# Kernel tuning notes

Hardware: AMD Instinct MI355X
Metric: run time of the kernel (lower is better)

## Reference

```python
import jax, jax.numpy as jnp
import numpy as np

K_NEIGHBORS = 3  # self.K in DSVDD


def setup_inputs() -> dict:
    key = jax.random.key(0)
    k1, k2 = jax.random.split(key)
    B, N, C = 16, 3136, 112   # batch, h*w patches, descriptor channels
    M = 3136                  # memory-bank size
    phi_p = jax.random.normal(k1, (B, N, C), dtype=jnp.float32)
    C_bank = jax.random.normal(k2, (C, M), dtype=jnp.float32)
    return {"phi_p": phi_p, "C_bank": C_bank, "h": 56}


def reference(phi_p, C_bank, h):
    # squared distances via ||phi||^2 + ||c||^2 - 2 phi.c  -> (B, N, M)
    features = jnp.sum(phi_p * phi_p, axis=2, keepdims=True)        # (B, N, 1)
    centers = jnp.sum(C_bank * C_bank, axis=0, keepdims=True)       # (1, M)
    f_c = 2.0 * jnp.einsum('bnc,cm->bnm', phi_p, C_bank)            # (B, N, M)
    dist = jnp.sqrt(features + centers - f_c)                        # (B, N, M)
    # K smallest distances (ascending, like torch.topk(largest=False))
    neg_topk, _ = jax.lax.top_k(-dist, K_NEIGHBORS)                  # (B, N, K)
    dist_k = -neg_topk
    # softmin over K, take weight of the nearest neighbor times its distance
    softmin0 = jax.nn.softmax(-dist_k, axis=-1)[:, :, 0]             # (B, N)
    score = softmin0 * dist_k[:, :, 0]                               # (B, N)
    B, N = score.shape
    w = N // h
    return score.reshape(B, 1, h, w)  # b c h w with c=1
```

## Files before the change

### kernel.cpp

```cpp
#include <hip/hip_runtime.h>
#include <stdint.h>


typedef short s16x8 __attribute__((ext_vector_type(8)));
typedef float fx4 __attribute__((ext_vector_type(4)));

#define M_TOT 3136
#define CC 112
#define NROWS 50176
#define N_TILES_TOT 50

__device__ __forceinline__ unsigned short f2bf(float x) {
  unsigned u = __float_as_uint(x);
  u += 0x7fffu + ((u >> 16) & 1u);
  return (unsigned short)(u >> 16);
}

__device__ __forceinline__ void async16(const void* g, void* l) {
  __builtin_amdgcn_global_load_lds(
      (const __attribute__((address_space(1))) unsigned int*)g,
      (__attribute__((address_space(3))) unsigned int*)l, 16, 0, 0);
}

#define INSERT3(T0, T1, T2, V)                                  \
  do {                                                          \
    const float _a0 = (T0), _a1 = (T1), _v = (V);               \
    (T0) = fmaxf(_a0, _v);                                      \
    (T1) = __builtin_amdgcn_fmed3f(_a0, _a1, _v);               \
    (T2) = __builtin_amdgcn_fmed3f(_a1, (T2), _v);              \
  } while (0)

__global__ __launch_bounds__(256) void dsvdd_prep(const float* __restrict__ Cb,
                                                  unsigned char* __restrict__ CT2) {
  const int tile = blockIdx.x;
  __shared__ float partial[256];
  __shared__ float c2s[64];
  const int tm = threadIdx.x & 63;
  const int seg = threadIdx.x >> 6;
  const int m = tile * 64 + tm;
  float ss = 0.f;
  if (m < M_TOT) {
    for (int k = seg * 28; k < seg * 28 + 28; ++k) {
      const float x = Cb[(size_t)k * M_TOT + m];
      ss += x * x;
    }
  }
  partial[threadIdx.x] = ss;
  __syncthreads();
  if (seg == 0) {
    const float c2 = partial[tm] + partial[64 + tm] + partial[128 + tm] + partial[192 + tm];
    c2s[tm] = (m < M_TOT) ? (-0.125f * c2) : -2500.0f;
  }
  __syncthreads();
#pragma unroll
  for (int it = 0; it < 4; ++it) {
    const int s = it * 256 + threadIdx.x;
    const int f = s >> 8;
    const int ks = (s >> 6) & 3;
    const int l = s & 63;
    const int mloc = f * 16 + (l & 15);
    const int mm = tile * 64 + mloc;
    const bool mv = (mm < M_TOT);
    const int k0 = ks * 32 + (l >> 4) * 8;
    float v[8];
#pragma unroll
    for (int j = 0; j < 8; ++j) {
      const int k = k0 + j;
      float x = 0.f;
      if (k < CC) x = mv ? Cb[(size_t)k * M_TOT + mm] : 0.f;
      else if (k < 116) x = c2s[mloc];
      v[j] = x;
    }
    uint4 pk;
    pk.x = (unsigned)f2bf(v[0]) | ((unsigned)f2bf(v[1]) << 16);
    pk.y = (unsigned)f2bf(v[2]) | ((unsigned)f2bf(v[3]) << 16);
    pk.z = (unsigned)f2bf(v[4]) | ((unsigned)f2bf(v[5]) << 16);
    pk.w = (unsigned)f2bf(v[6]) | ((unsigned)f2bf(v[7]) << 16);
    *(uint4*)(CT2 + (size_t)tile * 16384 + (size_t)s * 16) = pk;
  }
}

__global__ __launch_bounds__(256, 4) void dsvdd_stage1(const float* __restrict__ phi,
                                                       const unsigned char* __restrict__ CT2,
                                                       float* __restrict__ part,
                                                       float* __restrict__ featg, int nT) {
  __shared__ __align__(16) unsigned char lds[32768];
  float(*const mg)[8] = (float(*)[8])lds;

  const int t = threadIdx.x;
  const int lane = t & 63;
  const int w = t >> 6;
  const int g = w >> 1;
  const int h = w & 1;
  const int cq = lane & 15;
  const int kq = lane >> 4;
  const int c = blockIdx.y;
  const int tile0 = c * nT;
  const int bid = (int)blockIdx.x;
  const long rowBase = (long)bid * 128;
  const bool needF = (c == 0);

  {
    const int r = t >> 1;
    const int h2 = t & 1;
    const float* src = phi + (size_t)(rowBase + r) * CC + h2 * 56;
    unsigned char* const base = lds + ((r >> 4) * 4096);
    const int pcq = r & 15;
    float ss = 0.f;
#pragma unroll
    for (int j = 0; j < 7; ++j) {
      const int k0 = h2 * 56 + j * 8;
      const int ks = k0 >> 5;
      const int kqw = (k0 >> 3) & 3;
      const float4 a = *(const float4*)(src + j * 8);
      const float4 b = *(const float4*)(src + j * 8 + 4);
      ss += a.x * a.x + a.y * a.y + a.z * a.z + a.w * a.w;
      ss += b.x * b.x + b.y * b.y + b.z * b.z + b.w * b.w;
      uint4 pk;
      pk.x = (unsigned)f2bf(a.x) | ((unsigned)f2bf(a.y) << 16);
      pk.y = (unsigned)f2bf(a.z) | ((unsigned)f2bf(a.w) << 16);
      pk.z = (unsigned)f2bf(b.x) | ((unsigned)f2bf(b.y) << 16);
      pk.w = (unsigned)f2bf(b.z) | ((unsigned)f2bf(b.w) << 16);
      *(uint4*)(base + ks * 1024 + (kqw * 16 + pcq) * 16) = pk;
    }
    {
      uint4 pk;
      if (h2 == 0) { pk.x = 0x3f803f80u; pk.y = 0x3f803f80u; pk.z = 0u; pk.w = 0u; }
      else { pk.x = pk.y = pk.z = pk.w = 0u; }
      *(uint4*)(base + 3 * 1024 + ((2 + h2) * 16 + pcq) * 16) = pk;
    }
    ss += __shfl_xor(ss, 1);
    if (needF && h2 == 0) featg[rowBase + r] = ss;
  }
  __syncthreads();

  s16x8 bg[4][4];
#pragma unroll
  for (int ks = 0; ks < 4; ++ks)
#pragma unroll
    for (int pf = 0; pf < 4; ++pf)
      bg[ks][pf] = *(const s16x8*)(lds + ((g * 4 + pf) * 4 + ks) * 1024 + lane * 16);
  __syncthreads();

#define STAGE(BUF, TIDX)                                                        \
  do {                                                                          \
    const unsigned char* _g =                                                   \
        CT2 + (size_t)(TIDX)*16384 + w * 4096 + (size_t)lane * 16;              \
    unsigned char* _l = lds + (BUF)*16384 + w * 4096;                           \
    _Pragma("unroll") for (int i = 0; i < 4; ++i)                               \
        async16(_g + i * 1024, _l + i * 1024);                                  \
  } while (0)

#define COMPUTE(BUF)                                                            \
  do {                                                                          \
    const unsigned char* _rd = lds + (BUF)*16384 + h * 8192 + lane * 16;        \
    const fx4 _zz = {0.f, 0.f, 0.f, 0.f};                                       \
    _Pragma("unroll") for (int mf = 0; mf < 2; ++mf) {                          \
      s16x8 af[4];                                                              \
      _Pragma("unroll") for (int ks = 0; ks < 4; ++ks)                          \
          af[ks] = *(const s16x8*)(_rd + mf * 4096 + ks * 1024);                \
      fx4 acc[4];                                                               \
      _Pragma("unroll") for (int ks = 0; ks < 4; ++ks)                          \
          _Pragma("unroll") for (int pf = 0; pf < 4; ++pf)                      \
              acc[pf] = __builtin_amdgcn_mfma_f32_16x16x32_bf16(                \
                  af[ks], bg[ks][pf], (ks == 0) ? _zz : acc[pf], 0, 0, 0);      \
      _Pragma("unroll") for (int pf = 0; pf < 4; ++pf)                          \
          _Pragma("unroll") for (int rg = 0; rg < 4; ++rg)                      \
              INSERT3(t0[pf], t1[pf], t2[pf], acc[pf][rg]);                     \
    }                                                                           \
  } while (0)

#define FENCE() __builtin_amdgcn_sched_barrier(0)

  float t0[4], t1[4], t2[4];
#pragma unroll
  for (int pf = 0; pf < 4; ++pf) t0[pf] = t1[pf] = t2[pf] = -3.0e38f;

  {
    const int j0 = bid % nT;
    const int j1 = (bid + 1) % nT;
    STAGE(0, tile0 + j0);
    STAGE(1, tile0 + j1);
  }
  for (int tt = 0; tt < nT; ++tt) {
    if (tt + 1 < nT) {
      asm volatile("s_waitcnt vmcnt(4)" ::: "memory");
    } else {
      asm volatile("s_waitcnt vmcnt(0)" ::: "memory");
    }
    FENCE();
    __builtin_amdgcn_s_barrier();
    FENCE();
    COMPUTE(tt & 1);
    FENCE();
    __builtin_amdgcn_s_barrier();
    FENCE();
    if (tt + 2 < nT) STAGE(tt & 1, tile0 + (bid + tt + 2) % nT);
  }
#undef STAGE
#undef COMPUTE
#undef FENCE

#pragma unroll
  for (int pf = 0; pf < 4; ++pf) {
#pragma unroll
    for (int off = 16; off < 64; off <<= 1) {
      const float b0 = __shfl_xor(t0[pf], off);
      const float b1 = __shfl_xor(t1[pf], off);
      const float b2 = __shfl_xor(t2[pf], off);
      INSERT3(t0[pf], t1[pf], t2[pf], b0);
      INSERT3(t0[pf], t1[pf], t2[pf], b1);
      INSERT3(t0[pf], t1[pf], t2[pf], b2);
    }
  }
  __syncthreads();
  if (kq == 0) {
#pragma unroll
    for (int pf = 0; pf < 4; ++pf) {
      const int row = g * 64 + pf * 16 + cq;
      mg[row][h * 3 + 0] = t0[pf];
      mg[row][h * 3 + 1] = t1[pf];
      mg[row][h * 3 + 2] = t2[pf];
    }
  }
  __syncthreads();
  if (t < 128) {
    float s0 = mg[t][0], s1 = mg[t][1], s2 = mg[t][2];
    INSERT3(s0, s1, s2, mg[t][3]);
    INSERT3(s0, s1, s2, mg[t][4]);
    INSERT3(s0, s1, s2, mg[t][5]);
    float* dst = part + ((size_t)c * NROWS + rowBase + t) * 3;
    dst[0] = s0; dst[1] = s1; dst[2] = s2;
  }
}

__global__ __launch_bounds__(256) void dsvdd_stage2(const float* __restrict__ part,
                                                    const float* __restrict__ featg,
                                                    float* __restrict__ out, int S) {
  const int row = blockIdx.x * 256 + threadIdx.x;
  if (row >= NROWS) return;
  float s0 = -3.0e38f, s1 = -3.0e38f, s2 = -3.0e38f;
  for (int c = 0; c < S; ++c) {
    const float* p = part + ((size_t)c * NROWS + row) * 3;
    INSERT3(s0, s1, s2, p[0]);
    INSERT3(s0, s1, s2, p[1]);
    INSERT3(s0, s1, s2, p[2]);
  }
  const float feat = featg[row];
  const float d0 = sqrtf(fmaxf(feat - 2.f * s0, 0.f));
  const float d1 = sqrtf(fmaxf(feat - 2.f * s1, 0.f));
  const float d2 = sqrtf(fmaxf(feat - 2.f * s2, 0.f));
  const float w0 = 1.0f / (1.0f + __expf(d0 - d1) + __expf(d0 - d2));
  out[row] = w0 * d0;
}

extern "C" void kernel_launch(void* const* d_in, const int* in_sizes, int n_in,
                              void* d_out, int out_size, void* d_ws, size_t ws_size,
                              hipStream_t stream) {
  (void)in_sizes; (void)n_in; (void)out_size;
  const float* phi = (const float*)d_in[0];
  const float* Cb = (const float*)d_in[1];
  float* out = (float*)d_out;
  unsigned char* CT2 = (unsigned char*)d_ws;
  float* featg = (float*)((unsigned char*)d_ws + 819200);
  float* partp = (float*)((unsigned char*)d_ws + 819200 + 200704);
  const size_t base = 819200 + 200704;
  int S = 1;
  if (ws_size >= base + (size_t)5 * NROWS * 12) S = 5;
  else if (ws_size >= base + (size_t)2 * NROWS * 12) S = 2;
  const int nT = N_TILES_TOT / S;
  dsvdd_prep<<<50, 256, 0, stream>>>(Cb, CT2);
  dsvdd_stage1<<<dim3(392, S), 256, 0, stream>>>(phi, CT2, partp, featg, nT);
  dsvdd_stage2<<<196, 256, 0, stream>>>(partp, featg, out, S);
}
```

Before: 64.69 us.

## Switch distance GEMM to 32x32x16 bf16 MFMA with matching operand layout

```diff
diff --git a/kernel.cpp b/kernel.cpp
--- a/kernel.cpp
+++ b/kernel.cpp
@@ -3,7 +3,7 @@
 
 
 typedef short s16x8 __attribute__((ext_vector_type(8)));
-typedef float fx4 __attribute__((ext_vector_type(4)));
+typedef float f32x16 __attribute__((ext_vector_type(16)));
 
 #define M_TOT 3136
 #define CC 112
@@ -55,13 +55,13 @@
 #pragma unroll
   for (int it = 0; it < 4; ++it) {
     const int s = it * 256 + threadIdx.x;
-    const int f = s >> 8;
-    const int ks = (s >> 6) & 3;
+    const int f = s >> 9;
+    const int ks = (s >> 6) & 7;
     const int l = s & 63;
-    const int mloc = f * 16 + (l & 15);
+    const int mloc = f * 32 + (l & 31);
     const int mm = tile * 64 + mloc;
     const bool mv = (mm < M_TOT);
-    const int k0 = ks * 32 + (l >> 4) * 8;
+    const int k0 = ks * 16 + (l >> 5) * 8;
     float v[8];
 #pragma unroll
     for (int j = 0; j < 8; ++j) {
@@ -92,8 +92,6 @@
   const int w = t >> 6;
   const int g = w >> 1;
   const int h = w & 1;
-  const int cq = lane & 15;
-  const int kq = lane >> 4;
   const int c = blockIdx.y;
   const int tile0 = c * nT;
   const int bid = (int)blockIdx.x;
@@ -104,14 +102,14 @@
     const int r = t >> 1;
     const int h2 = t & 1;
     const float* src = phi + (size_t)(rowBase + r) * CC + h2 * 56;
-    unsigned char* const base = lds + ((r >> 4) * 4096);
-    const int pcq = r & 15;
+    unsigned char* const base = lds + ((r >> 5) * 8) * 1024;
+    const int col = r & 31;
     float ss = 0.f;
 #pragma unroll
     for (int j = 0; j < 7; ++j) {
       const int k0 = h2 * 56 + j * 8;
-      const int ks = k0 >> 5;
-      const int kqw = (k0 >> 3) & 3;
+      const int ks = k0 >> 4;
+      const int khalf = (k0 >> 3) & 1;
       const float4 a = *(const float4*)(src + j * 8);
       const float4 b = *(const float4*)(src + j * 8 + 4);
       ss += a.x * a.x + a.y * a.y + a.z * a.z + a.w * a.w;
@@ -121,25 +119,25 @@
       pk.y = (unsigned)f2bf(a.z) | ((unsigned)f2bf(a.w) << 16);
       pk.z = (unsigned)f2bf(b.x) | ((unsigned)f2bf(b.y) << 16);
       pk.w = (unsigned)f2bf(b.z) | ((unsigned)f2bf(b.w) << 16);
-      *(uint4*)(base + ks * 1024 + (kqw * 16 + pcq) * 16) = pk;
+      *(uint4*)(base + ks * 1024 + (khalf * 32 + col) * 16) = pk;
     }
     {
       uint4 pk;
       if (h2 == 0) { pk.x = 0x3f803f80u; pk.y = 0x3f803f80u; pk.z = 0u; pk.w = 0u; }
       else { pk.x = pk.y = pk.z = pk.w = 0u; }
-      *(uint4*)(base + 3 * 1024 + ((2 + h2) * 16 + pcq) * 16) = pk;
+      *(uint4*)(base + 7 * 1024 + ((h2 * 32) + col) * 16) = pk;
     }
     ss += __shfl_xor(ss, 1);
     if (needF && h2 == 0) featg[rowBase + r] = ss;
   }
   __syncthreads();
 
-  s16x8 bg[4][4];
-#pragma unroll
-  for (int ks = 0; ks < 4; ++ks)
-#pragma unroll
-    for (int pf = 0; pf < 4; ++pf)
-      bg[ks][pf] = *(const s16x8*)(lds + ((g * 4 + pf) * 4 + ks) * 1024 + lane * 16);
+  s16x8 bg0[8], bg1[8];
+#pragma unroll
+  for (int ks = 0; ks < 8; ++ks) {
+    bg0[ks] = *(const s16x8*)(lds + ((g * 2 + 0) * 8 + ks) * 1024 + lane * 16);
+    bg1[ks] = *(const s16x8*)(lds + ((g * 2 + 1) * 8 + ks) * 1024 + lane * 16);
+  }
   __syncthreads();
 
 #define STAGE(BUF, TIDX)                                                        \
@@ -154,33 +152,35 @@
 #define COMPUTE(BUF)                                                            \
   do {                                                                          \
     const unsigned char* _rd = lds + (BUF)*16384 + h * 8192 + lane * 16;        \
-    const fx4 _zz = {0.f, 0.f, 0.f, 0.f};                                       \
-    _Pragma("unroll") for (int mf = 0; mf < 2; ++mf) {                          \
-      s16x8 af[4];                                                              \
-      _Pragma("unroll") for (int ks = 0; ks < 4; ++ks)                          \
-          af[ks] = *(const s16x8*)(_rd + mf * 4096 + ks * 1024);                \
-      fx4 acc[4];                                                               \
-      _Pragma("unroll") for (int ks = 0; ks < 4; ++ks)                          \
-          _Pragma("unroll") for (int pf = 0; pf < 4; ++pf)                      \
-              acc[pf] = __builtin_amdgcn_mfma_f32_16x16x32_bf16(                \
-                  af[ks], bg[ks][pf], (ks == 0) ? _zz : acc[pf], 0, 0, 0);      \
-      _Pragma("unroll") for (int pf = 0; pf < 4; ++pf)                          \
-          _Pragma("unroll") for (int rg = 0; rg < 4; ++rg)                      \
-              INSERT3(t0[pf], t1[pf], t2[pf], acc[pf][rg]);                     \
+    s16x8 af[8];                                                                \
+    _Pragma("unroll") for (int ks = 0; ks < 8; ++ks)                            \
+        af[ks] = *(const s16x8*)(_rd + ks * 1024);                              \
+    f32x16 acc0, acc1;                                                          \
+    __builtin_amdgcn_s_setprio(1);                                              \
+    _Pragma("unroll") for (int ks = 0; ks < 8; ++ks) {                          \
+      acc0 = __builtin_amdgcn_mfma_f32_32x32x16_bf16(                           \
+          af[ks], bg0[ks], (ks == 0) ? (f32x16)0.f : acc0, 0, 0, 0);            \
+      acc1 = __builtin_amdgcn_mfma_f32_32x32x16_bf16(                           \
+          af[ks], bg1[ks], (ks == 0) ? (f32x16)0.f : acc1, 0, 0, 0);            \
+    }                                                                           \
+    __builtin_amdgcn_s_setprio(0);                                              \
+    _Pragma("unroll") for (int rg = 0; rg < 16; ++rg) {                         \
+      INSERT3(t00, t01, t02, acc0[rg]);                                         \
+      INSERT3(t10, t11, t12, acc1[rg]);                                         \
     }                                                                           \
   } while (0)
 
 #define FENCE() __builtin_amdgcn_sched_barrier(0)
 
-  float t0[4], t1[4], t2[4];
-#pragma unroll
-  for (int pf = 0; pf < 4; ++pf) t0[pf] = t1[pf] = t2[pf] = -3.0e38f;
-
-  {
-    const int j0 = bid % nT;
-    const int j1 = (bid + 1) % nT;
-    STAGE(0, tile0 + j0);
+  float t00, t01, t02, t10, t11, t12;
+  t00 = t01 = t02 = t10 = t11 = t12 = -3.0e38f;
+
+  int jst = bid % nT;
+  {
+    const int j1 = (jst + 1 < nT) ? jst + 1 : 0;
+    STAGE(0, tile0 + jst);
     STAGE(1, tile0 + j1);
+    jst = j1;
   }
   for (int tt = 0; tt < nT; ++tt) {
     if (tt + 1 < nT) {
@@ -195,33 +195,29 @@
     FENCE();
     __builtin_amdgcn_s_barrier();
     FENCE();
-    if (tt + 2 < nT) STAGE(tt & 1, tile0 + (bid + tt + 2) % nT);
+    if (tt + 2 < nT) {
+      jst = (jst + 1 < nT) ? jst + 1 : 0;
+      STAGE(tt & 1, tile0 + jst);
+    }
   }
 #undef STAGE
 #undef COMPUTE
 #undef FENCE
 
-#pragma unroll
-  for (int pf = 0; pf < 4; ++pf) {
-#pragma unroll
-    for (int off = 16; off < 64; off <<= 1) {
-      const float b0 = __shfl_xor(t0[pf], off);
-      const float b1 = __shfl_xor(t1[pf], off);
-      const float b2 = __shfl_xor(t2[pf], off);
-      INSERT3(t0[pf], t1[pf], t2[pf], b0);
-      INSERT3(t0[pf], t1[pf], t2[pf], b1);
-      INSERT3(t0[pf], t1[pf], t2[pf], b2);
-    }
-  }
-  __syncthreads();
-  if (kq == 0) {
-#pragma unroll
-    for (int pf = 0; pf < 4; ++pf) {
-      const int row = g * 64 + pf * 16 + cq;
-      mg[row][h * 3 + 0] = t0[pf];
-      mg[row][h * 3 + 1] = t1[pf];
-      mg[row][h * 3 + 2] = t2[pf];
-    }
+  {
+    const float b0 = __shfl_xor(t00, 32), b1 = __shfl_xor(t01, 32), b2 = __shfl_xor(t02, 32);
+    INSERT3(t00, t01, t02, b0); INSERT3(t00, t01, t02, b1); INSERT3(t00, t01, t02, b2);
+  }
+  {
+    const float b0 = __shfl_xor(t10, 32), b1 = __shfl_xor(t11, 32), b2 = __shfl_xor(t12, 32);
+    INSERT3(t10, t11, t12, b0); INSERT3(t10, t11, t12, b1); INSERT3(t10, t11, t12, b2);
+  }
+  __syncthreads();
+  if (lane < 32) {
+    const int row0 = g * 64 + lane;
+    const int row1 = g * 64 + 32 + lane;
+    mg[row0][h * 3 + 0] = t00; mg[row0][h * 3 + 1] = t01; mg[row0][h * 3 + 2] = t02;
+    mg[row1][h * 3 + 0] = t10; mg[row1][h * 3 + 1] = t11; mg[row1][h * 3 + 2] = t12;
   }
   __syncthreads();
   if (t < 128) {
```

Result: slower. 85.50 us (+32.2%).
